# Optimization experiments

Measured on AMD Instinct MI355X. Metric: run time of the kernel, lower is better.

Reference implementation:

```python
import jax, jax.numpy as jnp
import numpy as np

N_NODES = 100000
N_GRAPHS = 128

def _graph_conv(x, W, b, s, d, n_nodes):
    """DGL GraphConv with norm='both': D_dst^{-1/2} A D_src^{-1/2} X W + b."""
    ones = jnp.ones(s.shape[0], x.dtype)
    deg_out = jax.ops.segment_sum(ones, s, num_segments=n_nodes)  # src out-degree
    deg_in = jax.ops.segment_sum(ones, d, num_segments=n_nodes)   # dst in-degree
    norm_src = jnp.where(deg_out > 0, 1.0 / jnp.sqrt(jnp.maximum(deg_out, 1.0)), 0.0)
    norm_dst = jnp.where(deg_in > 0, 1.0 / jnp.sqrt(jnp.maximum(deg_in, 1.0)), 0.0)
    h = x * norm_src[:, None]                    # [N, F]
    agg = jax.ops.segment_sum(h[s], d, num_segments=n_nodes)  # SpMM gather-scatter
    rst = (agg @ W) * norm_dst[:, None] + b
    return rst

def _hetero_layer(x, Ws, bs, src, dst, n_nodes):
    # HeteroGraphConv aggregate='sum' over relations (fixed small set -> loop ok)
    out = jnp.zeros((n_nodes, Ws.shape[-1]), x.dtype)
    for r in range(Ws.shape[0]):
        out = out + _graph_conv(x, Ws[r], bs[r], src[r], dst[r], n_nodes)
    return out

def setup_inputs() -> dict:
    key = jax.random.key(0)
    ks = jax.random.split(key, 8)
    feat = jax.random.normal(ks[0], (N_NODES, 256), dtype=jnp.float32)
    src = jax.random.randint(ks[1], (3, 400000), 0, N_NODES)
    dst = jax.random.randint(ks[2], (3, 400000), 0, N_NODES)
    graph_ids = jnp.sort(jax.random.randint(ks[3], (N_NODES,), 0, N_GRAPHS))
    W1 = jax.random.normal(ks[4], (3, 256, 256), dtype=jnp.float32) * 0.06
    b1 = jnp.zeros((3, 256), dtype=jnp.float32)
    W2 = jax.random.normal(ks[5], (3, 256, 256), dtype=jnp.float32) * 0.06
    b2 = jnp.zeros((3, 256), dtype=jnp.float32)
    return {"feat": feat, "src": src, "dst": dst, "graph_ids": graph_ids,
            "W1": W1, "b1": b1, "W2": W2, "b2": b2}

def reference(feat, src, dst, graph_ids, W1, b1, W2, b2):
    n_nodes = feat.shape[0]
    h = _hetero_layer(feat, W1, b1, src, dst, n_nodes)
    h = jax.nn.relu(h)
    h = _hetero_layer(h, W2, b2, src, dst, n_nodes)
    # AvgPooling over batched graphs
    sums = jax.ops.segment_sum(h, graph_ids, num_segments=N_GRAPHS)
    counts = jax.ops.segment_sum(jnp.ones(n_nodes, h.dtype), graph_ids, num_segments=N_GRAPHS)
    return sums / jnp.maximum(counts, 1.0)[:, None]
```

## Files before the change

kernel.cpp:

```cpp
#include <hip/hip_runtime.h>
#include <stdint.h>

#define NN 100000
#define NE 400000
#define NR 3
#define NF 256
#define NK 768
#define NG 128
#define SCAN_NB ((NN + 1023) / 1024)

typedef __attribute__((ext_vector_type(4))) unsigned short ushortx4;
typedef __attribute__((ext_vector_type(8))) unsigned short ushortx8;
typedef __attribute__((ext_vector_type(8))) short short8;
typedef __attribute__((ext_vector_type(4))) float floatx4;

static __device__ __forceinline__ unsigned short f2bfu(float f) {
  union { float f; uint32_t u; } c; c.f = f;
  uint32_t x = c.u;
  uint32_t r = (x + 0x7fffu + ((x >> 16) & 1u)) >> 16;
  return (unsigned short)r;
}
static __device__ __forceinline__ float bfu2f(unsigned short u) {
  union { uint32_t u; float f; } c; c.u = ((uint32_t)u) << 16;
  return c.f;
}

static __device__ __forceinline__ void gload16(const void* g, void* l) {
  __builtin_amdgcn_global_load_lds(
      (const __attribute__((address_space(1))) uint32_t*)g,
      (__attribute__((address_space(3))) uint32_t*)l, 16, 0, 0);
}


__global__ __launch_bounds__(256) void degree_kernel(
    const int* __restrict__ src, const int* __restrict__ dst,
    int* __restrict__ deg_out, int* __restrict__ deg_in) {
  int t = blockIdx.x * 256 + threadIdx.x;
  int r = blockIdx.y;
  if (t < NE) {
    atomicAdd(&deg_out[r * NN + src[r * NE + t]], 1);
    atomicAdd(&deg_in[r * NN + dst[r * NE + t]], 1);
  }
}


__global__ __launch_bounds__(256) void scan_phaseA(
    const int* __restrict__ deg_in, int* __restrict__ blocksum) {
  int r = blockIdx.y, b = blockIdx.x, tid = threadIdx.x;
  const int* deg = deg_in + (size_t)r * NN;
  int base = b * 1024 + tid * 4;
  int s = 0;
#pragma unroll
  for (int i = 0; i < 4; ++i) { int idx = base + i; if (idx < NN) s += deg[idx]; }
  __shared__ int red[256];
  red[tid] = s; __syncthreads();
  for (int off = 128; off > 0; off >>= 1) {
    if (tid < off) red[tid] += red[tid + off];
    __syncthreads();
  }
  if (tid == 0) blocksum[r * SCAN_NB + b] = red[0];
}

__global__ __launch_bounds__(128) void scan_phaseB(
    int* __restrict__ blocksum, int* __restrict__ rowptr) {
  int r = blockIdx.x, tid = threadIdx.x;
  int* bs = blocksum + r * SCAN_NB;
  __shared__ int buf[128];
  int v = (tid < SCAN_NB) ? bs[tid] : 0;
  buf[tid] = v; __syncthreads();
  for (int off = 1; off < 128; off <<= 1) {
    int t = (tid >= off) ? buf[tid - off] : 0;
    __syncthreads();
    buf[tid] += t;
    __syncthreads();
  }
  if (tid < SCAN_NB) bs[tid] = buf[tid] - v;
  if (tid == 127) rowptr[(size_t)r * (NN + 1) + NN] = buf[127];
}

__global__ __launch_bounds__(256) void scan_phaseC(
    const int* __restrict__ deg_in, const int* __restrict__ blocksum,
    int* __restrict__ rowptr, float* __restrict__ n_dst) {
  int r = blockIdx.y, b = blockIdx.x, tid = threadIdx.x;
  const int* deg = deg_in + (size_t)r * NN;
  int* rp = rowptr + (size_t)r * (NN + 1);
  int base = b * 1024 + tid * 4;
  int v[4]; int s = 0;
#pragma unroll
  for (int i = 0; i < 4; ++i) { int idx = base + i; v[i] = (idx < NN) ? deg[idx] : 0; s += v[i]; }
  __shared__ int buf[256];
  buf[tid] = s; __syncthreads();
  for (int off = 1; off < 256; off <<= 1) {
    int t = (tid >= off) ? buf[tid - off] : 0;
    __syncthreads();
    buf[tid] += t;
    __syncthreads();
  }
  int excl = buf[tid] - s + blocksum[r * SCAN_NB + b];
#pragma unroll
  for (int i = 0; i < 4; ++i) {
    int idx = base + i;
    if (idx < NN) {
      rp[idx] = excl;
      n_dst[(size_t)r * NN + idx] = v[i] > 0 ? rsqrtf((float)v[i]) : 0.f;
    }
    excl += v[i];
  }
}

__global__ __launch_bounds__(256) void scatter_kernel(
    const int* __restrict__ src, const int* __restrict__ dst,
    int* __restrict__ cursor, const int* __restrict__ deg_out,
    int2* __restrict__ csr_e) {
  int t = blockIdx.x * 256 + threadIdx.x;
  int r = blockIdx.y;
  if (t < NE) {
    int s = src[r * NE + t], v = dst[r * NE + t];
    int pos = atomicAdd(&cursor[r * (NN + 1) + v], 1);
    float w = rsqrtf((float)deg_out[r * NN + s]);
    csr_e[(size_t)r * NE + pos] = make_int2(s, __float_as_int(w));
  }
}


__global__ __launch_bounds__(256) void prep_w_kernel(
    const float* __restrict__ W1, const float* __restrict__ W2,
    unsigned short* __restrict__ wt1, unsigned short* __restrict__ wt2) {
  __shared__ float lds[64][65];
  const int tile = blockIdx.x;
  const int r = blockIdx.y;
  const int lay = blockIdx.z;
  const float* W = lay ? W2 : W1;
  unsigned short* wt = lay ? wt2 : wt1;
  const int k0 = (tile >> 2) * 64, n0 = (tile & 3) * 64;
  const int ty = threadIdx.x >> 6;
  const int tx = threadIdx.x & 63;

#pragma unroll
  for (int i = 0; i < 16; ++i) {
    int kl = ty * 16 + i;
    lds[kl][tx] = W[((size_t)r * NF + k0 + kl) * NF + n0 + tx];
  }
  __syncthreads();
#pragma unroll
  for (int i = 0; i < 16; ++i) {
    int nl = ty * 16 + i;
    wt[(size_t)(n0 + nl) * NK + r * NF + k0 + tx] = f2bfu(lds[tx][nl]);
  }
}

__global__ __launch_bounds__(256) void prep_bias_kernel(
    const float* __restrict__ b1, const float* __restrict__ b2,
    float* __restrict__ bs1, float* __restrict__ bs2) {
  int t = blockIdx.x * 256 + threadIdx.x;
  if (t < 2 * NF) {
    int lay = t / NF, n = t % NF;
    const float* b = lay ? b2 : b1;
    float* bs = lay ? bs2 : bs1;
    bs[n] = b[n] + b[NF + n] + b[2 * NF + n];
  }
}

__global__ __launch_bounds__(256) void cast_kernel(
    const float* __restrict__ in, unsigned short* __restrict__ out, int n4) {
  int t = blockIdx.x * 256 + threadIdx.x;
  if (t < n4) {
    floatx4 v = __builtin_nontemporal_load((const floatx4*)&in[(size_t)t * 4]);
    ushortx4 o;
    o.x = f2bfu(v.x); o.y = f2bfu(v.y); o.z = f2bfu(v.z); o.w = f2bfu(v.w);
    *(ushortx4*)&out[(size_t)t * 4] = o;
  }
}


__global__ __launch_bounds__(256) void spmm_kernel(
    const unsigned short* __restrict__ x,
    const int* __restrict__ rowptr, const int2* __restrict__ csr_e,
    const float* __restrict__ n_dst,
    unsigned short* __restrict__ agg) {
  int wid = threadIdx.x >> 6, l = threadIdx.x & 63;
  int v = blockIdx.x * 4 + wid;
  if (v >= NN) return;
  const int half = l >> 5;
  const int c8 = (l & 31) * 8;

  int ea = rowptr[v],                e1a = rowptr[v + 1];
  int eb = rowptr[(NN + 1) + v],     e1b = rowptr[(NN + 1) + v + 1];
  int ec = rowptr[2 * (NN + 1) + v], e1c = rowptr[2 * (NN + 1) + v + 1];
  const int2* cea = csr_e;
  const int2* ceb = csr_e + (size_t)NE;
  const int2* cec = csr_e + (size_t)2 * NE;

  float a[NR][8];
#pragma unroll
  for (int r = 0; r < NR; ++r)
#pragma unroll
    for (int j = 0; j < 8; ++j) a[r][j] = 0.f;

  int2 qa = make_int2(0, 0), qb = make_int2(0, 0), qc = make_int2(0, 0);
  if (ea + half < e1a) qa = cea[ea + half];
  if (eb + half < e1b) qb = ceb[eb + half];
  if (ec + half < e1c) qc = cec[ec + half];

  while (ea < e1a || eb < e1b || ec < e1c) {
    int2 na = make_int2(0, 0), nb = make_int2(0, 0), nc = make_int2(0, 0);
    if (ea + 2 + half < e1a) na = cea[ea + 2 + half];
    if (eb + 2 + half < e1b) nb = ceb[eb + 2 + half];
    if (ec + 2 + half < e1c) nc = cec[ec + 2 + half];

    if (ea < e1a) {
      if (ea + half < e1a) {
        float w = __int_as_float(qa.y);
        ushortx8 xv = *(const ushortx8*)&x[(size_t)qa.x * NF + c8];
#pragma unroll
        for (int j = 0; j < 8; ++j) a[0][j] += w * bfu2f(xv[j]);
      }
      ea += 2; qa = na;
    }
    if (eb < e1b) {
      if (eb + half < e1b) {
        float w = __int_as_float(qb.y);
        ushortx8 xv = *(const ushortx8*)&x[(size_t)qb.x * NF + c8];
#pragma unroll
        for (int j = 0; j < 8; ++j) a[1][j] += w * bfu2f(xv[j]);
      }
      eb += 2; qb = nb;
    }
    if (ec < e1c) {
      if (ec + half < e1c) {
        float w = __int_as_float(qc.y);
        ushortx8 xv = *(const ushortx8*)&x[(size_t)qc.x * NF + c8];
#pragma unroll
        for (int j = 0; j < 8; ++j) a[2][j] += w * bfu2f(xv[j]);
      }
      ec += 2; qc = nc;
    }
  }

#pragma unroll
  for (int r = 0; r < NR; ++r)
#pragma unroll
    for (int j = 0; j < 8; ++j) a[r][j] += __shfl_xor(a[r][j], 32);

  if (l < 32) {
#pragma unroll
    for (int r = 0; r < NR; ++r) {
      float nd = n_dst[r * NN + v];
      ushortx8 o;
#pragma unroll
      for (int j = 0; j < 8; ++j) o[j] = f2bfu(a[r][j] * nd);
      *(ushortx8*)&agg[(size_t)v * NK + r * NF + c8] = o;
    }
  }
}


__global__ __launch_bounds__(256, 2) void gemm_kernel(
    const unsigned short* __restrict__ A,
    const unsigned short* __restrict__ Bt,
    const float* __restrict__ bias,
    unsigned short* __restrict__ C,
    int M, int relu) {
  __shared__ unsigned short ldsA[3][128 * 32];
  __shared__ unsigned short ldsB[2][256 * 32];
  const int tid = threadIdx.x;
  const int l = tid & 63, wid = tid >> 6;
  const int row0 = blockIdx.x * 128;
  const int c0 = wid * 64;

  floatx4 acc[8][4];
#pragma unroll
  for (int i = 0; i < 8; ++i)
#pragma unroll
    for (int j = 0; j < 4; ++j)
#pragma unroll
      for (int q = 0; q < 4; ++q) acc[i][j][q] = 0.f;

  const int fr = l & 15, fk = (l >> 4) * 8;

  auto stageA = [&](int b, int kt) {
    const int k0 = kt * 32;
    int u = wid * 64 + l;
    int arow = row0 + (u >> 2);
    if (arow >= M) arow = M - 1;
    gload16(A + (size_t)arow * NK + k0 + (u & 3) * 8, &ldsA[b][u * 8]);
    u += 256;
    arow = row0 + (u >> 2);
    if (arow >= M) arow = M - 1;
    gload16(A + (size_t)arow * NK + k0 + (u & 3) * 8, &ldsA[b][u * 8]);
  };
  auto stageB = [&](int b, int kt) {
    const int k0 = kt * 32;
#pragma unroll
    for (int p = 0; p < 4; ++p) {
      int uu = p * 256 + wid * 64 + l;
      gload16(Bt + (size_t)(uu >> 2) * NK + k0 + (uu & 3) * 8, &ldsB[b][uu * 8]);
    }
  };

  const int NKT = NK / 32;
  stageB(0, 0);
  stageA(0, 0);
  stageA(1, 1);

  for (int kt = 0; kt < NKT; ++kt) {
    if (kt < NKT - 1) {
      asm volatile("s_waitcnt vmcnt(2)" ::: "memory");
    } else {
      asm volatile("s_waitcnt vmcnt(0)" ::: "memory");
    }
    __builtin_amdgcn_s_barrier();
    __builtin_amdgcn_sched_barrier(0);

    if (kt + 1 < NKT) stageB((kt + 1) & 1, kt + 1);
    if (kt + 2 < NKT) stageA((kt + 2) % 3, kt + 2);
    __builtin_amdgcn_sched_barrier(0);

    const int ba = kt % 3, bb = kt & 1;
    short8 af[8], bf[4];
#pragma unroll
    for (int m = 0; m < 8; ++m)
      af[m] = *(const short8*)&ldsA[ba][(m * 16 + fr) * 32 + fk];
#pragma unroll
    for (int n = 0; n < 4; ++n)
      bf[n] = *(const short8*)&ldsB[bb][(c0 + n * 16 + fr) * 32 + fk];
#pragma unroll
    for (int m = 0; m < 8; ++m)
#pragma unroll
      for (int n = 0; n < 4; ++n)
        acc[m][n] = __builtin_amdgcn_mfma_f32_16x16x32_bf16(af[m], bf[n], acc[m][n], 0, 0, 0);
  }

  const int fq = l >> 4;
#pragma unroll
  for (int m = 0; m < 8; ++m) {
#pragma unroll
    for (int n = 0; n < 4; ++n) {
      int col = c0 + n * 16 + fr;
      float bv = bias[col];
#pragma unroll
      for (int q = 0; q < 4; ++q) {
        int row = row0 + m * 16 + fq * 4 + q;
        if (row < M) {
          float vv = acc[m][n][q] + bv;
          if (relu) vv = fmaxf(vv, 0.f);
          C[(size_t)row * NF + col] = f2bfu(vv);
        }
      }
    }
  }
}


__global__ __launch_bounds__(256) void pool_kernel(
    const unsigned short* __restrict__ h2, const int* __restrict__ gid,
    float* __restrict__ poolsum) {
  int c = threadIdx.x;
  int v0 = blockIdx.x * 256;
  int vend = min(v0 + 256, NN);
  float acc = 0.f;
  int curg = -1;
  for (int v = v0; v < vend; ++v) {
    int g = gid[v];
    if (g != curg) {
      if (curg >= 0) atomicAdd(&poolsum[curg * NF + c], acc);
      curg = g; acc = 0.f;
    }
    acc += bfu2f(h2[(size_t)v * NF + c]);
  }
  if (curg >= 0) atomicAdd(&poolsum[curg * NF + c], acc);
}

__global__ __launch_bounds__(256) void final_kernel(
    const float* __restrict__ poolsum, const int* __restrict__ gid,
    float* __restrict__ out) {
  int g = blockIdx.x, c = threadIdx.x;
  int lo = 0, hi = NN;
  while (lo < hi) { int mid = (lo + hi) >> 1; if (gid[mid] < g) lo = mid + 1; else hi = mid; }
  int a = lo;
  lo = 0; hi = NN;
  while (lo < hi) { int mid = (lo + hi) >> 1; if (gid[mid] < g + 1) lo = mid + 1; else hi = mid; }
  float cnt = (float)(lo - a);
  out[g * NF + c] = poolsum[g * NF + c] / fmaxf(cnt, 1.f);
}


extern "C" void kernel_launch(void* const* d_in, const int* in_sizes, int n_in,
                              void* d_out, int out_size, void* d_ws, size_t ws_size,
                              hipStream_t stream) {
  const float* feat = (const float*)d_in[0];
  const int* src = (const int*)d_in[1];
  const int* dst = (const int*)d_in[2];
  const int* gid = (const int*)d_in[3];
  const float* W1 = (const float*)d_in[4];
  const float* b1 = (const float*)d_in[5];
  const float* W2 = (const float*)d_in[6];
  const float* b2 = (const float*)d_in[7];
  float* out = (float*)d_out;

  char* ws = (char*)d_ws;
  size_t off = 0;
  auto alloc = [&](size_t bytes) -> void* {
    void* p = ws + off;
    off = (off + bytes + 255) & ~(size_t)255;
    return p;
  };

  int* deg_out = (int*)alloc((size_t)NR * NN * 4);
  int* deg_in  = (int*)alloc((size_t)NR * NN * 4);
  float* poolsum = (float*)alloc((size_t)NG * NF * 4);
  size_t zero_bytes = off;

  int* cursor  = (int*)alloc((size_t)NR * (NN + 1) * 4);
  int* blocksum = (int*)alloc((size_t)NR * SCAN_NB * 4);
  float* n_dst = (float*)alloc((size_t)NR * NN * 4);
  int* rowptr  = (int*)alloc((size_t)NR * (NN + 1) * 4);
  int2* csr_e  = (int2*)alloc((size_t)NR * NE * 8);
  unsigned short* wt1 = (unsigned short*)alloc((size_t)NF * NK * 2);
  unsigned short* wt2 = (unsigned short*)alloc((size_t)NF * NK * 2);
  float* bs1 = (float*)alloc(NF * 4);
  float* bs2 = (float*)alloc(NF * 4);
  unsigned short* featbf = (unsigned short*)alloc((size_t)NN * NF * 2);
  unsigned short* h1 = (unsigned short*)alloc((size_t)NN * NF * 2);
  unsigned short* h2 = (unsigned short*)alloc((size_t)NN * NF * 2);
  unsigned short* agg = (unsigned short*)alloc((size_t)NN * NK * 2);
  (void)ws_size; (void)in_sizes; (void)n_in; (void)out_size;

  hipMemsetAsync(d_ws, 0, zero_bytes, stream);

  dim3 eg((NE + 255) / 256, NR);
  degree_kernel<<<eg, 256, 0, stream>>>(src, dst, deg_out, deg_in);
  scan_phaseA<<<dim3(SCAN_NB, NR), 256, 0, stream>>>(deg_in, blocksum);
  scan_phaseB<<<NR, 128, 0, stream>>>(blocksum, rowptr);
  scan_phaseC<<<dim3(SCAN_NB, NR), 256, 0, stream>>>(deg_in, blocksum, rowptr, n_dst);
  hipMemcpyAsync(cursor, rowptr, (size_t)NR * (NN + 1) * 4,
                 hipMemcpyDeviceToDevice, stream);
  scatter_kernel<<<eg, 256, 0, stream>>>(src, dst, cursor, deg_out, csr_e);

  prep_w_kernel<<<dim3(16, NR, 2), 256, 0, stream>>>(W1, W2, wt1, wt2);
  prep_bias_kernel<<<2, 256, 0, stream>>>(b1, b2, bs1, bs2);
  cast_kernel<<<(NN * NF / 4 + 255) / 256, 256, 0, stream>>>(feat, featbf, NN * NF / 4);

  spmm_kernel<<<(NN + 3) / 4, 256, 0, stream>>>(featbf, rowptr, csr_e, n_dst, agg);
  gemm_kernel<<<(NN + 127) / 128, 256, 0, stream>>>(agg, wt1, bs1, h1, NN, 1);
  spmm_kernel<<<(NN + 3) / 4, 256, 0, stream>>>(h1, rowptr, csr_e, n_dst, agg);
  gemm_kernel<<<(NN + 127) / 128, 256, 0, stream>>>(agg, wt2, bs2, h2, NN, 0);
  pool_kernel<<<(NN + 255) / 256, 256, 0, stream>>>(h2, gid, poolsum);
  final_kernel<<<NG, 256, 0, stream>>>(poolsum, gid, out);
}
```

Before: 703.2 us.

## Make GEMM persistent with atomic tile scheduler and fuse pooling into one kernel

The GEMM becomes a persistent kernel: 512 blocks repeatedly fetch 128-row tiles from an atomic counter that is zeroed each call, instead of launching one block per tile. The aim is to cut launch and tail overhead across the 782 tiles. Pooling is also restructured so that each of 128 blocks finds its graph's node range by binary search and sums the rows directly, with no atomics. This removes the poolsum buffer and one kernel launch, but pooling now runs on only 128 blocks, and graph sizes may be uneven.

```diff
diff --git a/kernel.cpp b/kernel.cpp
--- a/kernel.cpp
+++ b/kernel.cpp
@@ -8,6 +8,7 @@
 #define NK 768
 #define NG 128
 #define SCAN_NB ((NN + 1023) / 1024)
+#define NT_GEMM ((NN + 127) / 128)
 
 typedef __attribute__((ext_vector_type(4))) unsigned short ushortx4;
 typedef __attribute__((ext_vector_type(8))) unsigned short ushortx8;
@@ -260,119 +261,108 @@
     const unsigned short* __restrict__ Bt,
     const float* __restrict__ bias,
     unsigned short* __restrict__ C,
-    int M, int relu) {
+    int M, int relu, int* __restrict__ tilectr) {
   __shared__ unsigned short ldsA[3][128 * 32];
   __shared__ unsigned short ldsB[2][256 * 32];
+  __shared__ int s_tile;
   const int tid = threadIdx.x;
   const int l = tid & 63, wid = tid >> 6;
-  const int row0 = blockIdx.x * 128;
   const int c0 = wid * 64;
-
-  floatx4 acc[8][4];
-#pragma unroll
-  for (int i = 0; i < 8; ++i)
-#pragma unroll
-    for (int j = 0; j < 4; ++j)
-#pragma unroll
-      for (int q = 0; q < 4; ++q) acc[i][j][q] = 0.f;
-
   const int fr = l & 15, fk = (l >> 4) * 8;
-
-  auto stageA = [&](int b, int kt) {
-    const int k0 = kt * 32;
-    int u = wid * 64 + l;
-    int arow = row0 + (u >> 2);
-    if (arow >= M) arow = M - 1;
-    gload16(A + (size_t)arow * NK + k0 + (u & 3) * 8, &ldsA[b][u * 8]);
-    u += 256;
-    arow = row0 + (u >> 2);
-    if (arow >= M) arow = M - 1;
-    gload16(A + (size_t)arow * NK + k0 + (u & 3) * 8, &ldsA[b][u * 8]);
-  };
-  auto stageB = [&](int b, int kt) {
-    const int k0 = kt * 32;
-#pragma unroll
-    for (int p = 0; p < 4; ++p) {
-      int uu = p * 256 + wid * 64 + l;
-      gload16(Bt + (size_t)(uu >> 2) * NK + k0 + (uu & 3) * 8, &ldsB[b][uu * 8]);
-    }
-  };
-
   const int NKT = NK / 32;
-  stageB(0, 0);
-  stageA(0, 0);
-  stageA(1, 1);
-
-  for (int kt = 0; kt < NKT; ++kt) {
-    if (kt < NKT - 1) {
-      asm volatile("s_waitcnt vmcnt(2)" ::: "memory");
-    } else {
-      asm volatile("s_waitcnt vmcnt(0)" ::: "memory");
-    }
-    __builtin_amdgcn_s_barrier();
-    __builtin_amdgcn_sched_barrier(0);
-
-    if (kt + 1 < NKT) stageB((kt + 1) & 1, kt + 1);
-    if (kt + 2 < NKT) stageA((kt + 2) % 3, kt + 2);
-    __builtin_amdgcn_sched_barrier(0);
-
-    const int ba = kt % 3, bb = kt & 1;
-    short8 af[8], bf[4];
-#pragma unroll
-    for (int m = 0; m < 8; ++m)
-      af[m] = *(const short8*)&ldsA[ba][(m * 16 + fr) * 32 + fk];
-#pragma unroll
-    for (int n = 0; n < 4; ++n)
-      bf[n] = *(const short8*)&ldsB[bb][(c0 + n * 16 + fr) * 32 + fk];
-#pragma unroll
-    for (int m = 0; m < 8; ++m)
+
+  for (;;) {
+    if (tid == 0) s_tile = atomicAdd(tilectr, 1);
+    __syncthreads();
+    const int tile = s_tile;
+    if (tile >= NT_GEMM) return;
+    const int row0 = tile * 128;
+
+    floatx4 acc[8][4];
+#pragma unroll
+    for (int i = 0; i < 8; ++i)
+#pragma unroll
+      for (int j = 0; j < 4; ++j)
+#pragma unroll
+        for (int q = 0; q < 4; ++q) acc[i][j][q] = 0.f;
+
+    auto stageA = [&](int b, int kt) {
+      const int k0 = kt * 32;
+      int u = wid * 64 + l;
+      int arow = row0 + (u >> 2);
+      if (arow >= M) arow = M - 1;
+      gload16(A + (size_t)arow * NK + k0 + (u & 3) * 8, &ldsA[b][u * 8]);
+      u += 256;
+      arow = row0 + (u >> 2);
+      if (arow >= M) arow = M - 1;
+      gload16(A + (size_t)arow * NK + k0 + (u & 3) * 8, &ldsA[b][u * 8]);
+    };
+    auto stageB = [&](int b, int kt) {
+      const int k0 = kt * 32;
+#pragma unroll
+      for (int p = 0; p < 4; ++p) {
+        int uu = p * 256 + wid * 64 + l;
+        gload16(Bt + (size_t)(uu >> 2) * NK + k0 + (uu & 3) * 8, &ldsB[b][uu * 8]);
+      }
+    };
+
+    stageB(0, 0);
+    stageA(0, 0);
+    stageA(1, 1);
+
+    for (int kt = 0; kt < NKT; ++kt) {
+      if (kt < NKT - 1) {
+        asm volatile("s_waitcnt vmcnt(2)" ::: "memory");
+      } else {
+        asm volatile("s_waitcnt vmcnt(0)" ::: "memory");
+      }
+      __builtin_amdgcn_s_barrier();
+      __builtin_amdgcn_sched_barrier(0);
+
+      if (kt + 1 < NKT) stageB((kt + 1) & 1, kt + 1);
+      if (kt + 2 < NKT) stageA((kt + 2) % 3, kt + 2);
+      __builtin_amdgcn_sched_barrier(0);
+
+      const int ba = kt % 3, bb = kt & 1;
+      short8 af[8], bf[4];
+#pragma unroll
+      for (int m = 0; m < 8; ++m)
+        af[m] = *(const short8*)&ldsA[ba][(m * 16 + fr) * 32 + fk];
 #pragma unroll
       for (int n = 0; n < 4; ++n)
-        acc[m][n] = __builtin_amdgcn_mfma_f32_16x16x32_bf16(af[m], bf[n], acc[m][n], 0, 0, 0);
-  }
-
-  const int fq = l >> 4;
-#pragma unroll
-  for (int m = 0; m < 8; ++m) {
-#pragma unroll
-    for (int n = 0; n < 4; ++n) {
-      int col = c0 + n * 16 + fr;
-      float bv = bias[col];
-#pragma unroll
-      for (int q = 0; q < 4; ++q) {
-        int row = row0 + m * 16 + fq * 4 + q;
-        if (row < M) {
-          float vv = acc[m][n][q] + bv;
-          if (relu) vv = fmaxf(vv, 0.f);
-          C[(size_t)row * NF + col] = f2bfu(vv);
+        bf[n] = *(const short8*)&ldsB[bb][(c0 + n * 16 + fr) * 32 + fk];
+#pragma unroll
+      for (int m = 0; m < 8; ++m)
+#pragma unroll
+        for (int n = 0; n < 4; ++n)
+          acc[m][n] = __builtin_amdgcn_mfma_f32_16x16x32_bf16(af[m], bf[n], acc[m][n], 0, 0, 0);
+    }
+
+    const int fq = l >> 4;
+#pragma unroll
+    for (int m = 0; m < 8; ++m) {
+#pragma unroll
+      for (int n = 0; n < 4; ++n) {
+        int col = c0 + n * 16 + fr;
+        float bv = bias[col];
+#pragma unroll
+        for (int q = 0; q < 4; ++q) {
+          int row = row0 + m * 16 + fq * 4 + q;
+          if (row < M) {
+            float vv = acc[m][n][q] + bv;
+            if (relu) vv = fmaxf(vv, 0.f);
+            C[(size_t)row * NF + col] = f2bfu(vv);
+          }
         }
       }
     }
+    __syncthreads();
   }
 }
 
 
 __global__ __launch_bounds__(256) void pool_kernel(
     const unsigned short* __restrict__ h2, const int* __restrict__ gid,
-    float* __restrict__ poolsum) {
-  int c = threadIdx.x;
-  int v0 = blockIdx.x * 256;
-  int vend = min(v0 + 256, NN);
-  float acc = 0.f;
-  int curg = -1;
-  for (int v = v0; v < vend; ++v) {
-    int g = gid[v];
-    if (g != curg) {
-      if (curg >= 0) atomicAdd(&poolsum[curg * NF + c], acc);
-      curg = g; acc = 0.f;
-    }
-    acc += bfu2f(h2[(size_t)v * NF + c]);
-  }
-  if (curg >= 0) atomicAdd(&poolsum[curg * NF + c], acc);
-}
-
-__global__ __launch_bounds__(256) void final_kernel(
-    const float* __restrict__ poolsum, const int* __restrict__ gid,
     float* __restrict__ out) {
   int g = blockIdx.x, c = threadIdx.x;
   int lo = 0, hi = NN;
@@ -380,8 +370,18 @@
   int a = lo;
   lo = 0; hi = NN;
   while (lo < hi) { int mid = (lo + hi) >> 1; if (gid[mid] < g + 1) lo = mid + 1; else hi = mid; }
-  float cnt = (float)(lo - a);
-  out[g * NF + c] = poolsum[g * NF + c] / fmaxf(cnt, 1.f);
+  int b = lo;
+  float acc = 0.f;
+  int v = a;
+  for (; v + 4 <= b; v += 4) {
+    float t0 = bfu2f(h2[(size_t)(v + 0) * NF + c]);
+    float t1 = bfu2f(h2[(size_t)(v + 1) * NF + c]);
+    float t2 = bfu2f(h2[(size_t)(v + 2) * NF + c]);
+    float t3 = bfu2f(h2[(size_t)(v + 3) * NF + c]);
+    acc += t0 + t1 + t2 + t3;
+  }
+  for (; v < b; ++v) acc += bfu2f(h2[(size_t)v * NF + c]);
+  out[g * NF + c] = acc / fmaxf((float)(b - a), 1.f);
 }
 
 
@@ -408,7 +408,7 @@
 
   int* deg_out = (int*)alloc((size_t)NR * NN * 4);
   int* deg_in  = (int*)alloc((size_t)NR * NN * 4);
-  float* poolsum = (float*)alloc((size_t)NG * NF * 4);
+  int* tilectr = (int*)alloc(2 * 4);
   size_t zero_bytes = off;
 
   int* cursor  = (int*)alloc((size_t)NR * (NN + 1) * 4);
@@ -442,9 +442,8 @@
   cast_kernel<<<(NN * NF / 4 + 255) / 256, 256, 0, stream>>>(feat, featbf, NN * NF / 4);
 
   spmm_kernel<<<(NN + 3) / 4, 256, 0, stream>>>(featbf, rowptr, csr_e, n_dst, agg);
-  gemm_kernel<<<(NN + 127) / 128, 256, 0, stream>>>(agg, wt1, bs1, h1, NN, 1);
+  gemm_kernel<<<512, 256, 0, stream>>>(agg, wt1, bs1, h1, NN, 1, tilectr);
   spmm_kernel<<<(NN + 3) / 4, 256, 0, stream>>>(h1, rowptr, csr_e, n_dst, agg);
-  gemm_kernel<<<(NN + 127) / 128, 256, 0, stream>>>(agg, wt2, bs2, h2, NN, 0);
-  pool_kernel<<<(NN + 255) / 256, 256, 0, stream>>>(h2, gid, poolsum);
-  final_kernel<<<NG, 256, 0, stream>>>(poolsum, gid, out);
-}
+  gemm_kernel<<<512, 256, 0, stream>>>(agg, wt2, bs2, h2, NN, 0, tilectr + 1);
+  pool_kernel<<<NG, 256, 0, stream>>>(h2, gid, out);
+}
```

Measured after the change: 705.2 us. About the same (+0.3%).
